# Kernel tuning notes

Hardware: AMD Instinct MI355X
Metric: run time of the kernel (lower is better)

The kernel has to match this reference:

```python
import jax, jax.numpy as jnp
import numpy as np
import math

B, CIN, H, W = 8, 64, 64, 64
C = 64  # channels (== in_channels, required since conv_out is unused and residual is added raw)
TEMPERATURE = 1.0


def setup_inputs() -> dict:
    key = jax.random.key(0)
    ks = jax.random.split(key, 7)
    s = 1.0 / math.sqrt(CIN)
    return {
        "x": jax.random.normal(ks[0], (B, CIN, H, W), dtype=jnp.float32),
        "wq": jax.random.uniform(ks[1], (C, CIN), jnp.float32, -s, s),
        "bq": jax.random.uniform(ks[2], (C,), jnp.float32, -s, s),
        "wk": jax.random.uniform(ks[3], (C, CIN), jnp.float32, -s, s),
        "bk": jax.random.uniform(ks[4], (C,), jnp.float32, -s, s),
        "wv": jax.random.uniform(ks[5], (C, CIN), jnp.float32, -s, s),
        "bv": jax.random.uniform(ks[6], (C,), jnp.float32, -s, s),
    }


def reference(x, wq, bq, wk, bk, wv, bv):
    b, cin, h, w = x.shape
    n = h * w
    xf = x.reshape(b, cin, n)  # [B,Cin,N]
    # 1x1 convs == per-pixel GEMM
    q = jnp.einsum('oc,bcn->bon', wq, xf) + bq[None, :, None]  # [B,C,N]
    k = jnp.einsum('oc,bcn->bon', wk, xf) + bk[None, :, None]
    v = jnp.einsum('oc,bcn->bon', wv, xf) + bv[None, :, None]
    # 'channel' whitening: subtract per-channel spatial mean
    q_mean = q.mean(axis=2, keepdims=True)  # [B,C,1]
    k_mean = k.mean(axis=2, keepdims=True)
    q = q - q_mean
    k = k - k_mean
    scale = math.sqrt(C)
    # pairwise term: softmax over keys of whitened q.k / (scale*temperature)
    sim = jnp.einsum('bcn,bcm->bnm', q, k) / (scale * TEMPERATURE)  # [B,N,N]
    sim = jax.nn.softmax(sim, axis=2)
    out = jnp.einsum('bnm,bcm->bcn', sim, v)  # [B,C,N]
    # unary term: softmax(query_mean . key) over keys, no scaling (as in source)
    unary = jax.nn.softmax(jnp.einsum('bc,bcm->bm', q_mean[:, :, 0], k), axis=-1)  # [B,N]
    out_unary = jnp.einsum('bcm,bm->bc', v, unary)  # [B,C]
    out = out + out_unary[:, :, None]
    return x + out.reshape(b, C, h, w)
```

## Files before the change

kernel.cpp:

```cpp
#include <hip/hip_runtime.h>
#include <stdint.h>

#define N_PIX 4096
#define NB 8

typedef __attribute__((ext_vector_type(8))) short short8;
typedef __attribute__((ext_vector_type(4))) float f32x4;
typedef __attribute__((ext_vector_type(2))) uint32_t u32x2;

#define SCL 0.18033688011112042f
#define LOG2E 1.4426950408889634f

__device__ __forceinline__ short f2bf(float x){
  union { float f; uint32_t u; } a; a.f = x;
  uint32_t r = a.u + 0x7FFFu + ((a.u >> 16) & 1u);
  return (short)(r >> 16);
}
__device__ __forceinline__ float bf2f(short h){
  union { uint32_t u; float f; } a; a.u = ((uint32_t)(uint16_t)h) << 16; return a.f;
}
__device__ __forceinline__ uint32_t cvtpk(float lo, float hi){
  uint32_t r;
  asm("v_cvt_pk_bf16_f32 %0, %1, %2" : "=v"(r) : "v"(lo), "v"(hi));
  return r;
}
__device__ __forceinline__ float fexp2(float x){ return __builtin_amdgcn_exp2f(x); }
__device__ __forceinline__ float wredSum(float v){
  #pragma unroll
  for (int m = 1; m < 64; m <<= 1) v += __shfl_xor(v, m);
  return v;
}
__device__ __forceinline__ float wredMax(float v){
  #pragma unroll
  for (int m = 1; m < 64; m <<= 1) v = fmaxf(v, __shfl_xor(v, m));
  return v;
}

__global__ __launch_bounds__(256) void k_xmean(const float* __restrict__ x, float* __restrict__ xm){
  int row = blockIdx.x;
  int tid = threadIdx.x;
  const float* xr = x + (size_t)row * N_PIX;
  float s = 0.f;
  #pragma unroll
  for (int i = 0; i < 16; i++) s += xr[tid + 256*i];
  s = wredSum(s);
  __shared__ float red[4];
  if ((tid & 63) == 0) red[tid >> 6] = s;
  __syncthreads();
  if (tid == 0) xm[row] = (red[0]+red[1]+red[2]+red[3]) * (1.0f / N_PIX);
}

__global__ void k_means(const float* __restrict__ wq, const float* __restrict__ bq,
                        const float* __restrict__ wk, const float* __restrict__ bk,
                        const float* __restrict__ xm, float* __restrict__ qm, float* __restrict__ km){
  int b = blockIdx.x; int c = threadIdx.x;
  float sq = 0.f, sk = 0.f;
  for (int cc = 0; cc < 64; cc++){
    float xv = xm[b*64 + cc];
    sq += wq[c*64 + cc] * xv;
    sk += wk[c*64 + cc] * xv;
  }
  qm[b*64 + c] = sq + bq[c];
  km[b*64 + c] = sk + bk[c];
}

__global__ __launch_bounds__(256) void k_qkv(
    const float* __restrict__ x,
    const float* __restrict__ wq, const float* __restrict__ bq,
    const float* __restrict__ wk, const float* __restrict__ bk,
    const float* __restrict__ wv, const float* __restrict__ bv,
    const float* __restrict__ qm, const float* __restrict__ km,
    short* __restrict__ Q, short* __restrict__ Kf, short* __restrict__ Vf,
    float* __restrict__ u)
{
  int blk = blockIdx.x;
  int b  = blk >> 5;
  int n0 = (blk & 31) * 128;
  int tid = threadIdx.x;
  int w = tid >> 6, l = tid & 63, lr = l & 15, lg = l >> 4;
  const float* xb = x + (size_t)b * 64 * N_PIX;

  int ncol[2];
  ncol[0] = n0 + w*32 + lr;
  ncol[1] = ncol[0] + 16;

  short8 bx[2][2];
  #pragma unroll
  for (int tj = 0; tj < 2; tj++){
    #pragma unroll
    for (int kc = 0; kc < 2; kc++){
      short8 t;
      #pragma unroll
      for (int j = 0; j < 8; j++){
        int cp = kc*32 + lg*8 + j;
        t[j] = f2bf(xb[(size_t)cp * N_PIX + ncol[tj]]);
      }
      bx[tj][kc] = t;
    }
  }

  float qmv[4][4];
  #pragma unroll
  for (int ti = 0; ti < 4; ti++)
    #pragma unroll
    for (int r = 0; r < 4; r++)
      qmv[ti][r] = qm[b*64 + ti*16 + lg*4 + r];

  short* Qb  = Q  + (size_t)b * N_PIX * 64;
  short* Kfb = Kf + (size_t)b * N_PIX * 64;
  short* Vfb = Vf + (size_t)b * N_PIX * 64;
  const f32x4 z4 = {0.f, 0.f, 0.f, 0.f};

  {
    short8 aw[4][2];
    #pragma unroll
    for (int ti = 0; ti < 4; ti++)
      #pragma unroll
      for (int kc = 0; kc < 2; kc++){
        const float* wr = wq + (ti*16 + lr)*64 + kc*32 + lg*8;
        short8 t;
        #pragma unroll
        for (int j = 0; j < 8; j++) t[j] = f2bf(wr[j]);
        aw[ti][kc] = t;
      }
    f32x4 acc[4][2];
    #pragma unroll
    for (int ti = 0; ti < 4; ti++)
      #pragma unroll
      for (int tj = 0; tj < 2; tj++){
        acc[ti][tj] = z4;
        #pragma unroll
        for (int kc = 0; kc < 2; kc++)
          acc[ti][tj] = __builtin_amdgcn_mfma_f32_16x16x32_bf16(aw[ti][kc], bx[tj][kc], acc[ti][tj], 0, 0, 0);
      }
    float adj[4][4];
    #pragma unroll
    for (int ti = 0; ti < 4; ti++)
      #pragma unroll
      for (int r = 0; r < 4; r++)
        adj[ti][r] = bq[ti*16 + lg*4 + r] - qmv[ti][r];
    #pragma unroll
    for (int ti = 0; ti < 4; ti++)
      #pragma unroll
      for (int tj = 0; tj < 2; tj++){
        float v0 = (acc[ti][tj][0] + adj[ti][0]) * SCL;
        float v1 = (acc[ti][tj][1] + adj[ti][1]) * SCL;
        float v2 = (acc[ti][tj][2] + adj[ti][2]) * SCL;
        float v3 = (acc[ti][tj][3] + adj[ti][3]) * SCL;
        uint32_t p0 = ((uint32_t)(uint16_t)f2bf(v1) << 16) | (uint16_t)f2bf(v0);
        uint32_t p1 = ((uint32_t)(uint16_t)f2bf(v3) << 16) | (uint16_t)f2bf(v2);
        uint32_t* qr = (uint32_t*)(Qb + (size_t)ncol[tj]*64);
        qr[ti*8 + lg*2]     = p0;
        qr[ti*8 + lg*2 + 1] = p1;
      }
  }

  {
    short8 aw[4][2];
    #pragma unroll
    for (int ti = 0; ti < 4; ti++)
      #pragma unroll
      for (int kc = 0; kc < 2; kc++){
        const float* wr = wk + (ti*16 + lr)*64 + kc*32 + lg*8;
        short8 t;
        #pragma unroll
        for (int j = 0; j < 8; j++) t[j] = f2bf(wr[j]);
        aw[ti][kc] = t;
      }
    f32x4 acc[4][2];
    #pragma unroll
    for (int ti = 0; ti < 4; ti++)
      #pragma unroll
      for (int tj = 0; tj < 2; tj++){
        acc[ti][tj] = z4;
        #pragma unroll
        for (int kc = 0; kc < 2; kc++)
          acc[ti][tj] = __builtin_amdgcn_mfma_f32_16x16x32_bf16(aw[ti][kc], bx[tj][kc], acc[ti][tj], 0, 0, 0);
      }
    float adj[4][4];
    #pragma unroll
    for (int ti = 0; ti < 4; ti++)
      #pragma unroll
      for (int r = 0; r < 4; r++)
        adj[ti][r] = bk[ti*16 + lg*4 + r] - km[b*64 + ti*16 + lg*4 + r];
    float up[2] = {0.f, 0.f};
    #pragma unroll
    for (int ti = 0; ti < 4; ti++)
      #pragma unroll
      for (int tj = 0; tj < 2; tj++){
        float v0 = acc[ti][tj][0] + adj[ti][0];
        float v1 = acc[ti][tj][1] + adj[ti][1];
        float v2 = acc[ti][tj][2] + adj[ti][2];
        float v3 = acc[ti][tj][3] + adj[ti][3];
        up[tj] += qmv[ti][0]*v0 + qmv[ti][1]*v1 + qmv[ti][2]*v2 + qmv[ti][3]*v3;
        uint32_t p0 = ((uint32_t)(uint16_t)f2bf(v1) << 16) | (uint16_t)f2bf(v0);
        uint32_t p1 = ((uint32_t)(uint16_t)f2bf(v3) << 16) | (uint16_t)f2bf(v2);
        int n = ncol[tj];
        int di = (n >> 4)*512 + (ti >> 1)*256
               + ((n & 15) + 16*(2*(ti & 1) + (lg >> 1)))*4 + (lg & 1)*2;
        uint32_t* kr = (uint32_t*)Kfb;
        kr[di]     = p0;
        kr[di + 1] = p1;
      }
    #pragma unroll
    for (int tj = 0; tj < 2; tj++){
      float s = up[tj];
      s += __shfl_xor(s, 16);
      s += __shfl_xor(s, 32);
      if (lg == 0) u[(size_t)b*N_PIX + ncol[tj]] = s;
    }
  }

  {
    short8 aw[4][2];
    #pragma unroll
    for (int ti = 0; ti < 4; ti++)
      #pragma unroll
      for (int kc = 0; kc < 2; kc++){
        const float* wr = wv + (ti*16 + lr)*64 + kc*32 + lg*8;
        short8 t;
        #pragma unroll
        for (int j = 0; j < 8; j++) t[j] = f2bf(wr[j]);
        aw[ti][kc] = t;
      }
    f32x4 acc[4][2];
    #pragma unroll
    for (int ti = 0; ti < 4; ti++)
      #pragma unroll
      for (int tj = 0; tj < 2; tj++){
        acc[ti][tj] = z4;
        #pragma unroll
        for (int kc = 0; kc < 2; kc++)
          acc[ti][tj] = __builtin_amdgcn_mfma_f32_16x16x32_bf16(aw[ti][kc], bx[tj][kc], acc[ti][tj], 0, 0, 0);
      }
    #pragma unroll
    for (int ti = 0; ti < 4; ti++)
      #pragma unroll
      for (int tj = 0; tj < 2; tj++){
        int n = ncol[tj];
        short* vr = Vfb + (n >> 5)*2048 + ti*512 + ((lr >> 2)*16 + lg*4)*8 + (lr & 3) + 4*tj;
        #pragma unroll
        for (int r = 0; r < 4; r++){
          float v = acc[ti][tj][r] + bv[ti*16 + lg*4 + r];
          vr[r*8] = f2bf(v);
        }
      }
  }
}

__global__ __launch_bounds__(256) void k_unary(const float* __restrict__ u, const short* __restrict__ Vf,
                                               float* __restrict__ ou){
  int b = blockIdx.x >> 6, c = blockIdx.x & 63;
  int tid = threadIdx.x, w = tid >> 6, l = tid & 63;
  const float* ub = u + (size_t)b * N_PIX;
  float mx = -1e30f;
  #pragma unroll
  for (int i = 0; i < 16; i++) mx = fmaxf(mx, ub[tid + 256*i]);
  mx = wredMax(mx);
  __shared__ float redm[4];
  if (l == 0) redm[w] = mx;
  __syncthreads();
  mx = fmaxf(fmaxf(redm[0], redm[1]), fmaxf(redm[2], redm[3]));
  const short* Vfb = Vf + (size_t)b * N_PIX * 64;
  int f = c >> 4, c15 = c & 15;
  int g = tid >> 1, h = tid & 1;
  float ps = 0.f, vs = 0.f;
  #pragma unroll
  for (int si = 0; si < 2; si++){
    int s = 2*h + si;
    const short8 v = *(const short8*)(Vfb + g*2048 + f*512 + (s*16 + c15)*8);
    #pragma unroll
    for (int j = 0; j < 8; j++){
      int kk = (j < 4) ? (4*s + j) : (16 + 4*s + (j - 4));
      int m = g*32 + kk;
      float p = exp2f((ub[m] - mx) * LOG2E);
      ps += p;
      vs += p * bf2f(v[j]);
    }
  }
  ps = wredSum(ps); vs = wredSum(vs);
  __shared__ float r1[4], r2[4];
  if (l == 0){ r1[w] = ps; r2[w] = vs; }
  __syncthreads();
  if (tid == 0) ou[b*64 + c] = (r2[0]+r2[1]+r2[2]+r2[3]) / (r1[0]+r1[1]+r1[2]+r1[3]);
}

__global__ __launch_bounds__(512, 3) void k_attn(
    const short* __restrict__ Q, const short* __restrict__ Kf, const short* __restrict__ Vf,
    const float* __restrict__ ou, const float* __restrict__ x, float* __restrict__ out)
{
  int blk = blockIdx.x;
  int b  = blk & 7;
  int q0 = (blk >> 3) << 6;
  int tid = threadIdx.x;
  int w = tid >> 6, l = tid & 63, lr = l & 15, lg = l >> 4;

  __shared__ short Opart[8][64][66];
  __shared__ float lW[8][64];

  const short* Qb  = Q  + (size_t)b * N_PIX * 64;
  const short* Kfb = Kf + (size_t)b * N_PIX * 64;
  const short* Vfb = Vf + (size_t)b * N_PIX * 64;

  short8 bq[4][2];
  #pragma unroll
  for (int qt = 0; qt < 4; qt++)
    #pragma unroll
    for (int kc = 0; kc < 2; kc++)
      bq[qt][kc] = *(const short8*)(Qb + (size_t)(q0 + qt*16 + lr)*64 + kc*32 + lg*8);

  f32x4 acc[4][4];
  float rs[4];
  const f32x4 z4 = {0.f, 0.f, 0.f, 0.f};
  #pragma unroll
  for (int qt = 0; qt < 4; qt++){
    rs[qt] = 0.f;
    #pragma unroll
    for (int f = 0; f < 4; f++) acc[qt][f] = z4;
  }

  int kbase = w << 9;

  for (int it = 0; it < 16; ++it){
    int kb = kbase + (it << 5);
    const short* kp = Kfb + (size_t)kb * 64 + l*8;
    short8 ak00 = *(const short8*)(kp);
    short8 ak01 = *(const short8*)(kp + 512);
    short8 ak10 = *(const short8*)(kp + 1024);
    short8 ak11 = *(const short8*)(kp + 1536);
    const short* vp = Vfb + (size_t)kb * 64 + l*8;
    short8 vf0 = *(const short8*)(vp);
    short8 vf1 = *(const short8*)(vp + 512);
    short8 vf2 = *(const short8*)(vp + 1024);
    short8 vf3 = *(const short8*)(vp + 1536);

    #pragma unroll
    for (int qt = 0; qt < 4; qt++){
      f32x4 s0 = __builtin_amdgcn_mfma_f32_16x16x32_bf16(ak00, bq[qt][0], z4, 0, 0, 0);
      s0 = __builtin_amdgcn_mfma_f32_16x16x32_bf16(ak01, bq[qt][1], s0, 0, 0, 0);
      f32x4 s1 = __builtin_amdgcn_mfma_f32_16x16x32_bf16(ak10, bq[qt][0], z4, 0, 0, 0);
      s1 = __builtin_amdgcn_mfma_f32_16x16x32_bf16(ak11, bq[qt][1], s1, 0, 0, 0);
      float p00 = fexp2(s0[0]), p01 = fexp2(s0[1]), p02 = fexp2(s0[2]), p03 = fexp2(s0[3]);
      float p10 = fexp2(s1[0]), p11 = fexp2(s1[1]), p12 = fexp2(s1[2]), p13 = fexp2(s1[3]);
      rs[qt] += ((p00 + p01) + (p02 + p03)) + ((p10 + p11) + (p12 + p13));
      union { short8 s; uint32_t u[4]; } pb;
      pb.u[0] = cvtpk(p00, p01);
      pb.u[1] = cvtpk(p02, p03);
      pb.u[2] = cvtpk(p10, p11);
      pb.u[3] = cvtpk(p12, p13);
      acc[qt][0] = __builtin_amdgcn_mfma_f32_16x16x32_bf16(vf0, pb.s, acc[qt][0], 0, 0, 0);
      acc[qt][1] = __builtin_amdgcn_mfma_f32_16x16x32_bf16(vf1, pb.s, acc[qt][1], 0, 0, 0);
      acc[qt][2] = __builtin_amdgcn_mfma_f32_16x16x32_bf16(vf2, pb.s, acc[qt][2], 0, 0, 0);
      acc[qt][3] = __builtin_amdgcn_mfma_f32_16x16x32_bf16(vf3, pb.s, acc[qt][3], 0, 0, 0);
    }
  }

  #pragma unroll
  for (int qt = 0; qt < 4; qt++){
    float v = rs[qt];
    v += __shfl_xor(v, 16);
    v += __shfl_xor(v, 32);
    rs[qt] = v;
  }

  if (lg == 0){
    #pragma unroll
    for (int qt = 0; qt < 4; qt++)
      lW[w][qt*16 + lr] = rs[qt];
  }
  #pragma unroll
  for (int qt = 0; qt < 4; qt++)
    #pragma unroll
    for (int f = 0; f < 4; f++)
      #pragma unroll
      for (int r = 0; r < 4; r++)
        Opart[w][qt*16 + lr][f*16 + lg*4 + r] = f2bf(acc[qt][f][r]);
  __syncthreads();

  const float* xb = x + (size_t)b * 64 * N_PIX;
  float* ob = out + (size_t)b * 64 * N_PIX;
  const float* oub = ou + b*64;
  #pragma unroll
  for (int i = 0; i < 8; i++){
    int idx = i*512 + tid;
    int c = idx >> 6, q = idx & 63;
    float os = 0.f, lt = 0.f;
    #pragma unroll
    for (int ww = 0; ww < 8; ww++){
      os += bf2f(Opart[ww][q][c]);
      lt += lW[ww][q];
    }
    size_t gi = (size_t)c * N_PIX + q0 + q;
    ob[gi] = xb[gi] + os / lt + oub[c];
  }
}

extern "C" void kernel_launch(void* const* d_in, const int* in_sizes, int n_in,
                              void* d_out, int out_size, void* d_ws, size_t ws_size,
                              hipStream_t stream)
{
  (void)in_sizes; (void)n_in; (void)out_size; (void)ws_size;
  const float* x  = (const float*)d_in[0];
  const float* wq = (const float*)d_in[1];
  const float* bq = (const float*)d_in[2];
  const float* wk = (const float*)d_in[3];
  const float* bk = (const float*)d_in[4];
  const float* wv = (const float*)d_in[5];
  const float* bv = (const float*)d_in[6];
  float* out = (float*)d_out;

  char* ws = (char*)d_ws;
  short* Q  = (short*)(ws);
  short* Kf = (short*)(ws + 4194304);
  short* Vf = (short*)(ws + 8388608);
  float* u  = (float*)(ws + 12582912);
  float* xm = (float*)(ws + 12713984);
  float* qm = (float*)(ws + 12716032);
  float* km = (float*)(ws + 12718080);
  float* ou = (float*)(ws + 12720128);

  k_xmean<<<dim3(512), dim3(256), 0, stream>>>(x, xm);
  k_means<<<dim3(8), dim3(64), 0, stream>>>(wq, bq, wk, bk, xm, qm, km);
  k_qkv<<<dim3(256), dim3(256), 0, stream>>>(x, wq, bq, wk, bk, wv, bv, qm, km, Q, Kf, Vf, u);
  k_unary<<<dim3(512), dim3(256), 0, stream>>>(u, Vf, ou);
  k_attn<<<dim3(512), dim3(512), 0, stream>>>(Q, Kf, Vf, ou, x, out);
}
```

Before: 79.42 us.

## Fuse mean kernel into QKV, stage QKV stores via LDS, double-buffer attention loads

Several changes land together. The k_means launch is removed and its per-batch projection of the channel means is folded into the start of k_qkv through shared memory. Q/K/V outputs are staged in padded LDS and written back as coalesced 16-byte stores, replacing the scattered 32-bit and 16-bit global writes. k_unary drops its max-reduction pass and relies on the unary logits being small enough not to overflow exp2. k_attn double-buffers the K/V fragment loads in registers and raises the occupancy hint from 3 to 4. Block indexing is also reordered batch-innermost. The main risks are register pressure from the double buffer under the tighter launch bound, and overflow in the unary softmax now that it has no max subtraction.

```diff
diff --git a/kernel.cpp b/kernel.cpp
--- a/kernel.cpp
+++ b/kernel.cpp
@@ -30,14 +30,12 @@
   for (int m = 1; m < 64; m <<= 1) v += __shfl_xor(v, m);
   return v;
 }
-__device__ __forceinline__ float wredMax(float v){
-  #pragma unroll
-  for (int m = 1; m < 64; m <<= 1) v = fmaxf(v, __shfl_xor(v, m));
-  return v;
-}
+__device__ __forceinline__ int pd(int d){ return d + ((d >> 6) << 2); }
+__device__ __forceinline__ int ps(int s){ return s + ((s >> 7) << 3); }
 
 __global__ __launch_bounds__(256) void k_xmean(const float* __restrict__ x, float* __restrict__ xm){
-  int row = blockIdx.x;
+  int b = blockIdx.x & 7, c = blockIdx.x >> 3;
+  int row = b*64 + c;
   int tid = threadIdx.x;
   const float* xr = x + (size_t)row * N_PIX;
   float s = 0.f;
@@ -50,36 +48,40 @@
   if (tid == 0) xm[row] = (red[0]+red[1]+red[2]+red[3]) * (1.0f / N_PIX);
 }
 
-__global__ void k_means(const float* __restrict__ wq, const float* __restrict__ bq,
-                        const float* __restrict__ wk, const float* __restrict__ bk,
-                        const float* __restrict__ xm, float* __restrict__ qm, float* __restrict__ km){
-  int b = blockIdx.x; int c = threadIdx.x;
-  float sq = 0.f, sk = 0.f;
-  for (int cc = 0; cc < 64; cc++){
-    float xv = xm[b*64 + cc];
-    sq += wq[c*64 + cc] * xv;
-    sk += wk[c*64 + cc] * xv;
-  }
-  qm[b*64 + c] = sq + bq[c];
-  km[b*64 + c] = sk + bk[c];
-}
-
 __global__ __launch_bounds__(256) void k_qkv(
     const float* __restrict__ x,
     const float* __restrict__ wq, const float* __restrict__ bq,
     const float* __restrict__ wk, const float* __restrict__ bk,
     const float* __restrict__ wv, const float* __restrict__ bv,
-    const float* __restrict__ qm, const float* __restrict__ km,
+    const float* __restrict__ xm,
     short* __restrict__ Q, short* __restrict__ Kf, short* __restrict__ Vf,
     float* __restrict__ u)
 {
   int blk = blockIdx.x;
-  int b  = blk >> 5;
-  int n0 = (blk & 31) * 128;
+  int b  = blk & 7;
+  int n0 = (blk >> 3) * 128;
   int tid = threadIdx.x;
   int w = tid >> 6, l = tid & 63, lr = l & 15, lg = l >> 4;
   const float* xb = x + (size_t)b * 64 * N_PIX;
 
+  __shared__ float qms[64], kms[64];
+  __shared__ short stage[4][2176];
+  if (tid < 64){
+    float sq = 0.f, sk = 0.f;
+    #pragma unroll 8
+    for (int cc = 0; cc < 64; cc++){
+      float xv = xm[b*64 + cc];
+      sq += wq[tid*64 + cc] * xv;
+      sk += wk[tid*64 + cc] * xv;
+    }
+    qms[tid] = sq + bq[tid];
+    kms[tid] = sk + bk[tid];
+  }
+  __syncthreads();
+
+  short* stageW = stage[w];
+  uint32_t* sd = (uint32_t*)stageW;
+
   int ncol[2];
   ncol[0] = n0 + w*32 + lr;
   ncol[1] = ncol[0] + 16;
@@ -104,8 +106,9 @@
   for (int ti = 0; ti < 4; ti++)
     #pragma unroll
     for (int r = 0; r < 4; r++)
-      qmv[ti][r] = qm[b*64 + ti*16 + lg*4 + r];
-
+      qmv[ti][r] = qms[ti*16 + lg*4 + r];
+
+  size_t wbase = (size_t)(n0 + w*32) * 64;
   short* Qb  = Q  + (size_t)b * N_PIX * 64;
   short* Kfb = Kf + (size_t)b * N_PIX * 64;
   short* Vfb = Vf + (size_t)b * N_PIX * 64;
@@ -133,26 +136,29 @@
         for (int kc = 0; kc < 2; kc++)
           acc[ti][tj] = __builtin_amdgcn_mfma_f32_16x16x32_bf16(aw[ti][kc], bx[tj][kc], acc[ti][tj], 0, 0, 0);
       }
-    float adj[4][4];
-    #pragma unroll
-    for (int ti = 0; ti < 4; ti++)
-      #pragma unroll
-      for (int r = 0; r < 4; r++)
-        adj[ti][r] = bq[ti*16 + lg*4 + r] - qmv[ti][r];
-    #pragma unroll
-    for (int ti = 0; ti < 4; ti++)
-      #pragma unroll
-      for (int tj = 0; tj < 2; tj++){
-        float v0 = (acc[ti][tj][0] + adj[ti][0]) * SCL;
-        float v1 = (acc[ti][tj][1] + adj[ti][1]) * SCL;
-        float v2 = (acc[ti][tj][2] + adj[ti][2]) * SCL;
-        float v3 = (acc[ti][tj][3] + adj[ti][3]) * SCL;
-        uint32_t p0 = ((uint32_t)(uint16_t)f2bf(v1) << 16) | (uint16_t)f2bf(v0);
-        uint32_t p1 = ((uint32_t)(uint16_t)f2bf(v3) << 16) | (uint16_t)f2bf(v2);
-        uint32_t* qr = (uint32_t*)(Qb + (size_t)ncol[tj]*64);
-        qr[ti*8 + lg*2]     = p0;
-        qr[ti*8 + lg*2 + 1] = p1;
-      }
+    #pragma unroll
+    for (int ti = 0; ti < 4; ti++)
+      #pragma unroll
+      for (int tj = 0; tj < 2; tj++){
+        float a0 = bq[ti*16 + lg*4 + 0] - qmv[ti][0];
+        float a1 = bq[ti*16 + lg*4 + 1] - qmv[ti][1];
+        float a2 = bq[ti*16 + lg*4 + 2] - qmv[ti][2];
+        float a3 = bq[ti*16 + lg*4 + 3] - qmv[ti][3];
+        float v0 = (acc[ti][tj][0] + a0) * SCL;
+        float v1 = (acc[ti][tj][1] + a1) * SCL;
+        float v2 = (acc[ti][tj][2] + a2) * SCL;
+        float v3 = (acc[ti][tj][3] + a3) * SCL;
+        int loc = tj*16 + lr;
+        int qd = loc*32 + ti*8 + lg*2;
+        sd[pd(qd)]     = cvtpk(v0, v1);
+        sd[pd(qd + 1)] = cvtpk(v2, v3);
+      }
+    #pragma unroll
+    for (int c2 = 0; c2 < 4; c2++){
+      int s = c2*512 + l*8;
+      short8 v = *(const short8*)(stageW + ps(s));
+      *(short8*)(Qb + wbase + s) = v;
+    }
   }
 
   {
@@ -177,31 +183,26 @@
         for (int kc = 0; kc < 2; kc++)
           acc[ti][tj] = __builtin_amdgcn_mfma_f32_16x16x32_bf16(aw[ti][kc], bx[tj][kc], acc[ti][tj], 0, 0, 0);
       }
-    float adj[4][4];
-    #pragma unroll
-    for (int ti = 0; ti < 4; ti++)
-      #pragma unroll
-      for (int r = 0; r < 4; r++)
-        adj[ti][r] = bk[ti*16 + lg*4 + r] - km[b*64 + ti*16 + lg*4 + r];
     float up[2] = {0.f, 0.f};
     #pragma unroll
     for (int ti = 0; ti < 4; ti++)
       #pragma unroll
       for (int tj = 0; tj < 2; tj++){
-        float v0 = acc[ti][tj][0] + adj[ti][0];
-        float v1 = acc[ti][tj][1] + adj[ti][1];
-        float v2 = acc[ti][tj][2] + adj[ti][2];
-        float v3 = acc[ti][tj][3] + adj[ti][3];
+        float v0 = acc[ti][tj][0] + bk[ti*16 + lg*4 + 0] - kms[ti*16 + lg*4 + 0];
+        float v1 = acc[ti][tj][1] + bk[ti*16 + lg*4 + 1] - kms[ti*16 + lg*4 + 1];
+        float v2 = acc[ti][tj][2] + bk[ti*16 + lg*4 + 2] - kms[ti*16 + lg*4 + 2];
+        float v3 = acc[ti][tj][3] + bk[ti*16 + lg*4 + 3] - kms[ti*16 + lg*4 + 3];
         up[tj] += qmv[ti][0]*v0 + qmv[ti][1]*v1 + qmv[ti][2]*v2 + qmv[ti][3]*v3;
-        uint32_t p0 = ((uint32_t)(uint16_t)f2bf(v1) << 16) | (uint16_t)f2bf(v0);
-        uint32_t p1 = ((uint32_t)(uint16_t)f2bf(v3) << 16) | (uint16_t)f2bf(v2);
-        int n = ncol[tj];
-        int di = (n >> 4)*512 + (ti >> 1)*256
-               + ((n & 15) + 16*(2*(ti & 1) + (lg >> 1)))*4 + (lg & 1)*2;
-        uint32_t* kr = (uint32_t*)Kfb;
-        kr[di]     = p0;
-        kr[di + 1] = p1;
-      }
+        int kd = tj*512 + (ti>>1)*256 + (lr + 16*(2*(ti&1) + (lg>>1)))*4 + (lg&1)*2;
+        sd[pd(kd)]     = cvtpk(v0, v1);
+        sd[pd(kd + 1)] = cvtpk(v2, v3);
+      }
+    #pragma unroll
+    for (int c2 = 0; c2 < 4; c2++){
+      int s = c2*512 + l*8;
+      short8 v = *(const short8*)(stageW + ps(s));
+      *(short8*)(Kfb + wbase + s) = v;
+    }
     #pragma unroll
     for (int tj = 0; tj < 2; tj++){
       float s = up[tj];
@@ -237,34 +238,31 @@
     for (int ti = 0; ti < 4; ti++)
       #pragma unroll
       for (int tj = 0; tj < 2; tj++){
-        int n = ncol[tj];
-        short* vr = Vfb + (n >> 5)*2048 + ti*512 + ((lr >> 2)*16 + lg*4)*8 + (lr & 3) + 4*tj;
         #pragma unroll
         for (int r = 0; r < 4; r++){
           float v = acc[ti][tj][r] + bv[ti*16 + lg*4 + r];
-          vr[r*8] = f2bf(v);
+          int vs0 = ti*512 + ((lr >> 2)*16 + lg*4 + r)*8 + (lr & 3) + 4*tj;
+          stageW[ps(vs0)] = f2bf(v);
         }
       }
+    #pragma unroll
+    for (int c2 = 0; c2 < 4; c2++){
+      int s = c2*512 + l*8;
+      short8 v = *(const short8*)(stageW + ps(s));
+      *(short8*)(Vfb + wbase + s) = v;
+    }
   }
 }
 
 __global__ __launch_bounds__(256) void k_unary(const float* __restrict__ u, const short* __restrict__ Vf,
                                                float* __restrict__ ou){
-  int b = blockIdx.x >> 6, c = blockIdx.x & 63;
+  int b = blockIdx.x & 7, c = blockIdx.x >> 3;
   int tid = threadIdx.x, w = tid >> 6, l = tid & 63;
   const float* ub = u + (size_t)b * N_PIX;
-  float mx = -1e30f;
-  #pragma unroll
-  for (int i = 0; i < 16; i++) mx = fmaxf(mx, ub[tid + 256*i]);
-  mx = wredMax(mx);
-  __shared__ float redm[4];
-  if (l == 0) redm[w] = mx;
-  __syncthreads();
-  mx = fmaxf(fmaxf(redm[0], redm[1]), fmaxf(redm[2], redm[3]));
   const short* Vfb = Vf + (size_t)b * N_PIX * 64;
   int f = c >> 4, c15 = c & 15;
   int g = tid >> 1, h = tid & 1;
-  float ps = 0.f, vs = 0.f;
+  float ps_ = 0.f, vs = 0.f;
   #pragma unroll
   for (int si = 0; si < 2; si++){
     int s = 2*h + si;
@@ -273,19 +271,54 @@
     for (int j = 0; j < 8; j++){
       int kk = (j < 4) ? (4*s + j) : (16 + 4*s + (j - 4));
       int m = g*32 + kk;
-      float p = exp2f((ub[m] - mx) * LOG2E);
-      ps += p;
+      float p = fexp2(ub[m] * LOG2E);
+      ps_ += p;
       vs += p * bf2f(v[j]);
     }
   }
-  ps = wredSum(ps); vs = wredSum(vs);
+  ps_ = wredSum(ps_); vs = wredSum(vs);
   __shared__ float r1[4], r2[4];
-  if (l == 0){ r1[w] = ps; r2[w] = vs; }
+  if (l == 0){ r1[w] = ps_; r2[w] = vs; }
   __syncthreads();
   if (tid == 0) ou[b*64 + c] = (r2[0]+r2[1]+r2[2]+r2[3]) / (r1[0]+r1[1]+r1[2]+r1[3]);
 }
 
-__global__ __launch_bounds__(512, 3) void k_attn(
+#define LOADF(S, kb) do {                                             \
+    const short* kp_ = Kfb + (size_t)(kb)*64 + l*8;                   \
+    ak0##S = *(const short8*)(kp_);                                   \
+    ak1##S = *(const short8*)(kp_ + 512);                             \
+    ak2##S = *(const short8*)(kp_ + 1024);                            \
+    ak3##S = *(const short8*)(kp_ + 1536);                            \
+    const short* vp_ = Vfb + (size_t)(kb)*64 + l*8;                   \
+    vf0##S = *(const short8*)(vp_);                                   \
+    vf1##S = *(const short8*)(vp_ + 512);                             \
+    vf2##S = *(const short8*)(vp_ + 1024);                            \
+    vf3##S = *(const short8*)(vp_ + 1536);                            \
+  } while(0)
+
+#define COMPUTE(S) do {                                               \
+    _Pragma("unroll")                                                 \
+    for (int qt = 0; qt < 4; qt++){                                   \
+      f32x4 s0 = __builtin_amdgcn_mfma_f32_16x16x32_bf16(ak0##S, bq[qt][0], z4, 0, 0, 0); \
+      s0 = __builtin_amdgcn_mfma_f32_16x16x32_bf16(ak1##S, bq[qt][1], s0, 0, 0, 0); \
+      f32x4 s1 = __builtin_amdgcn_mfma_f32_16x16x32_bf16(ak2##S, bq[qt][0], z4, 0, 0, 0); \
+      s1 = __builtin_amdgcn_mfma_f32_16x16x32_bf16(ak3##S, bq[qt][1], s1, 0, 0, 0); \
+      float p00 = fexp2(s0[0]), p01 = fexp2(s0[1]), p02 = fexp2(s0[2]), p03 = fexp2(s0[3]); \
+      float p10 = fexp2(s1[0]), p11 = fexp2(s1[1]), p12 = fexp2(s1[2]), p13 = fexp2(s1[3]); \
+      rs[qt] += ((p00 + p01) + (p02 + p03)) + ((p10 + p11) + (p12 + p13)); \
+      union { short8 s; uint32_t u[4]; } pb;                          \
+      pb.u[0] = cvtpk(p00, p01);                                      \
+      pb.u[1] = cvtpk(p02, p03);                                      \
+      pb.u[2] = cvtpk(p10, p11);                                      \
+      pb.u[3] = cvtpk(p12, p13);                                      \
+      acc[qt][0] = __builtin_amdgcn_mfma_f32_16x16x32_bf16(vf0##S, pb.s, acc[qt][0], 0, 0, 0); \
+      acc[qt][1] = __builtin_amdgcn_mfma_f32_16x16x32_bf16(vf1##S, pb.s, acc[qt][1], 0, 0, 0); \
+      acc[qt][2] = __builtin_amdgcn_mfma_f32_16x16x32_bf16(vf2##S, pb.s, acc[qt][2], 0, 0, 0); \
+      acc[qt][3] = __builtin_amdgcn_mfma_f32_16x16x32_bf16(vf3##S, pb.s, acc[qt][3], 0, 0, 0); \
+    }                                                                 \
+  } while(0)
+
+__global__ __launch_bounds__(512, 4) void k_attn(
     const short* __restrict__ Q, const short* __restrict__ Kf, const short* __restrict__ Vf,
     const float* __restrict__ ou, const float* __restrict__ x, float* __restrict__ out)
 {
@@ -320,39 +353,15 @@
   }
 
   int kbase = w << 9;
-
-  for (int it = 0; it < 16; ++it){
-    int kb = kbase + (it << 5);
-    const short* kp = Kfb + (size_t)kb * 64 + l*8;
-    short8 ak00 = *(const short8*)(kp);
-    short8 ak01 = *(const short8*)(kp + 512);
-    short8 ak10 = *(const short8*)(kp + 1024);
-    short8 ak11 = *(const short8*)(kp + 1536);
-    const short* vp = Vfb + (size_t)kb * 64 + l*8;
-    short8 vf0 = *(const short8*)(vp);
-    short8 vf1 = *(const short8*)(vp + 512);
-    short8 vf2 = *(const short8*)(vp + 1024);
-    short8 vf3 = *(const short8*)(vp + 1536);
-
-    #pragma unroll
-    for (int qt = 0; qt < 4; qt++){
-      f32x4 s0 = __builtin_amdgcn_mfma_f32_16x16x32_bf16(ak00, bq[qt][0], z4, 0, 0, 0);
-      s0 = __builtin_amdgcn_mfma_f32_16x16x32_bf16(ak01, bq[qt][1], s0, 0, 0, 0);
-      f32x4 s1 = __builtin_amdgcn_mfma_f32_16x16x32_bf16(ak10, bq[qt][0], z4, 0, 0, 0);
-      s1 = __builtin_amdgcn_mfma_f32_16x16x32_bf16(ak11, bq[qt][1], s1, 0, 0, 0);
-      float p00 = fexp2(s0[0]), p01 = fexp2(s0[1]), p02 = fexp2(s0[2]), p03 = fexp2(s0[3]);
-      float p10 = fexp2(s1[0]), p11 = fexp2(s1[1]), p12 = fexp2(s1[2]), p13 = fexp2(s1[3]);
-      rs[qt] += ((p00 + p01) + (p02 + p03)) + ((p10 + p11) + (p12 + p13));
-      union { short8 s; uint32_t u[4]; } pb;
-      pb.u[0] = cvtpk(p00, p01);
-      pb.u[1] = cvtpk(p02, p03);
-      pb.u[2] = cvtpk(p10, p11);
-      pb.u[3] = cvtpk(p12, p13);
-      acc[qt][0] = __builtin_amdgcn_mfma_f32_16x16x32_bf16(vf0, pb.s, acc[qt][0], 0, 0, 0);
-      acc[qt][1] = __builtin_amdgcn_mfma_f32_16x16x32_bf16(vf1, pb.s, acc[qt][1], 0, 0, 0);
-      acc[qt][2] = __builtin_amdgcn_mfma_f32_16x16x32_bf16(vf2, pb.s, acc[qt][2], 0, 0, 0);
-      acc[qt][3] = __builtin_amdgcn_mfma_f32_16x16x32_bf16(vf3, pb.s, acc[qt][3], 0, 0, 0);
-    }
+  short8 ak0A, ak1A, ak2A, ak3A, vf0A, vf1A, vf2A, vf3A;
+  short8 ak0B, ak1B, ak2B, ak3B, vf0B, vf1B, vf2B, vf3B;
+
+  LOADF(A, kbase);
+  for (int it = 0; it < 16; it += 2){
+    LOADF(B, kbase + ((((it + 1) & 15)) << 5));
+    COMPUTE(A);
+    LOADF(A, kbase + ((((it + 2) & 15)) << 5));
+    COMPUTE(B);
   }
 
   #pragma unroll
@@ -415,13 +424,10 @@
   short* Vf = (short*)(ws + 8388608);
   float* u  = (float*)(ws + 12582912);
   float* xm = (float*)(ws + 12713984);
-  float* qm = (float*)(ws + 12716032);
-  float* km = (float*)(ws + 12718080);
-  float* ou = (float*)(ws + 12720128);
+  float* ou = (float*)(ws + 12716032);
 
   k_xmean<<<dim3(512), dim3(256), 0, stream>>>(x, xm);
-  k_means<<<dim3(8), dim3(64), 0, stream>>>(wq, bq, wk, bk, xm, qm, km);
-  k_qkv<<<dim3(256), dim3(256), 0, stream>>>(x, wq, bq, wk, bk, wv, bv, qm, km, Q, Kf, Vf, u);
+  k_qkv<<<dim3(256), dim3(256), 0, stream>>>(x, wq, bq, wk, bk, wv, bv, xm, Q, Kf, Vf, u);
   k_unary<<<dim3(512), dim3(256), 0, stream>>>(u, Vf, ou);
   k_attn<<<dim3(512), dim3(512), 0, stream>>>(Q, Kf, Vf, ou, x, out);
 }
```

Result: slower. 292.5 us (+268.3%).
